# Kernel optimization log

Measured on AMD Instinct MI355X. Metric: run time of the kernel, lower is better.

Reference implementation:

```python
import jax, jax.numpy as jnp
import numpy as np

N_HEADS = 16
ROPE_THETA = 10000.0


def _rope(x):
    # x: (b, h, t, d). Interleaved-pair rotary embedding (lucidrains
    # rotary_embedding_torch convention: rotate_half on (d r) pairs, r=2).
    b, h, t, d = x.shape
    inv_freq = 1.0 / (ROPE_THETA ** (jnp.arange(0, d, 2, dtype=jnp.float32) / d))  # (d/2,)
    ang = jnp.arange(t, dtype=jnp.float32)[:, None] * inv_freq[None, :]            # (t, d/2)
    cos = jnp.cos(ang)
    sin = jnp.sin(ang)
    xp = x.reshape(b, h, t, d // 2, 2)
    x1, x2 = xp[..., 0], xp[..., 1]
    o1 = x1 * cos - x2 * sin
    o2 = x1 * sin + x2 * cos
    return jnp.stack([o1, o2], axis=-1).reshape(b, h, t, d)


def setup_inputs() -> dict:
    key = jax.random.key(0)
    k1, k2, k3 = jax.random.split(key, 3)
    B, T, C = 4, 2048, 1024
    x = jax.random.normal(k1, (B, T, C), dtype=jnp.float32)
    # torch nn.Linear weight layout: (out_features, in_features)
    w_attn = jax.random.normal(k2, (3 * C, C), dtype=jnp.float32) * (1.0 / np.sqrt(C))
    w_proj = jax.random.normal(k3, (C, C), dtype=jnp.float32) * (1.0 / np.sqrt(C))
    return {"x": x, "w_attn": w_attn, "w_proj": w_proj}


def reference(x, w_attn, w_proj):
    B, T, C = x.shape
    H = N_HEADS
    D = C // H
    # fused QKV projection: (b, t, 3C)
    qkv = jnp.einsum('btc,fc->btf', x, w_attn)
    # rearrange 'b t (r h d) -> r b h t d'
    qkv = qkv.reshape(B, T, 3, H, D).transpose(2, 0, 3, 1, 4)
    q, k, v = qkv[0], qkv[1], qkv[2]
    q = _rope(q)
    k = _rope(k)
    scale = 1.0 / np.sqrt(D).astype(np.float32)
    scores = jnp.einsum('bhqd,bhkd->bhqk', q, k) * scale
    attn = jax.nn.softmax(scores, axis=-1)
    y = jnp.einsum('bhqk,bhkd->bhqd', attn, v)       # (b, h, t, d)
    y = y.transpose(0, 2, 1, 3).reshape(B, T, C)     # 'b h t d -> b t (h d)'
    return jnp.einsum('btc,oc->bto', y, w_proj)
```

## Files before the change

### kernel.cpp

```cpp
#include <hip/hip_runtime.h>
#include <hip/hip_bf16.h>
#include <math.h>

typedef __bf16 bf16;
typedef float f32x4 __attribute__((ext_vector_type(4)));
typedef float f32x16 __attribute__((ext_vector_type(16)));
typedef bf16 bf16x8 __attribute__((ext_vector_type(8)));
typedef bf16 bf16x4 __attribute__((ext_vector_type(4)));
typedef unsigned int uint;
typedef uint uintx2 __attribute__((ext_vector_type(2)));

#define MFMA16(a, b, c) __builtin_amdgcn_mfma_f32_16x16x32_bf16(a, b, c, 0, 0, 0)
#define MFMA32(a, b, c) __builtin_amdgcn_mfma_f32_32x32x16_bf16(a, b, c, 0, 0, 0)

static constexpr int T_SEQ = 2048;
static constexpr int CDIM  = 1024;
static constexpr int NH    = 16;
static constexpr int DH    = 64;
static constexpr float FREQ_C = 0.20762050593045998f;
static constexpr float Q_SCALE = 0.18033688011112042f;

__device__ __forceinline__ float fexp2(float x) {
    return __builtin_amdgcn_exp2f(x);
}

__device__ __forceinline__ uint pack_bf16(float lo, float hi) {
    union { bf16 h[2]; uint u; } cv;
    cv.h[0] = (bf16)lo;
    cv.h[1] = (bf16)hi;
    return cv.u;
}

__device__ __forceinline__ void gld_lds16(const bf16* g, bf16* l) {
    __builtin_amdgcn_global_load_lds(
        (const __attribute__((address_space(1))) void*)g,
        (__attribute__((address_space(3))) void*)l, 16, 0, 0);
}

__device__ __forceinline__ void fast_sincos(float x, float* s, float* c) {
    const float INV2PI = 0.15915494309189535f;
    const float PI2_HI = 6.28125f;
    const float PI2_LO = 1.9353071795864769e-3f;
    const float n = rintf(x * INV2PI);
    float r = fmaf(-n, PI2_HI, x);
    r = fmaf(-n, PI2_LO, r);
    *s = __sinf(r);
    *c = __cosf(r);
}

__global__ __launch_bounds__(256)
void rope_table(float2* __restrict__ tab) {
    const int i = blockIdx.x * 256 + threadIdx.x;
    const int t = i >> 5, p = i & 31;
    const float ang = (float)t * exp2f(-2.0f * (float)p * FREQ_C);
    float s, c;
    fast_sincos(ang, &s, &c);
    tab[i] = make_float2(c, s);
}

__global__ __launch_bounds__(256)
void cvt_f32_bf16(const float* __restrict__ in, bf16* __restrict__ out, int n8) {
    const int i = blockIdx.x * 256 + threadIdx.x;
    if (i >= n8) return;
    const f32x4* p = (const f32x4*)(in + (size_t)i * 8);
    const f32x4 lo = p[0], hi = p[1];
    bf16x8 o;
    o[0] = (bf16)lo[0]; o[1] = (bf16)lo[1]; o[2] = (bf16)lo[2]; o[3] = (bf16)lo[3];
    o[4] = (bf16)hi[0]; o[5] = (bf16)hi[1]; o[6] = (bf16)hi[2]; o[7] = (bf16)hi[3];
    *(bf16x8*)(out + (size_t)i * 8) = o;
}

#define GEMM_CORE(Abase, Bbase, KDIM)                                            \
    f32x4 acc[4][4] = {};                                                        \
    for (int kk = 0; kk < (KDIM); kk += 64) {                                    \
        __syncthreads();                                                         \
        _Pragma("unroll")                                                        \
        for (int u = 0; u < 4; u++) {                                            \
            const int st = wave * 4 + u, mg = st >> 1, kg = st & 1;              \
            gld_lds16(Abase + (size_t)(mg * 16 + sm) * (KDIM) + kk + kg * 32 + sc * 8, \
                      &ash[st * 512]);                                           \
            gld_lds16(Bbase + (size_t)(mg * 16 + sm) * (KDIM) + kk + kg * 32 + sc * 8, \
                      &bsh[st * 512]);                                           \
        }                                                                        \
        __syncthreads();                                                         \
        _Pragma("unroll")                                                        \
        for (int kg = 0; kg < 2; kg++) {                                         \
            bf16x8 af[4], bfr[4];                                                \
            _Pragma("unroll")                                                    \
            for (int a = 0; a < 4; a++)                                          \
                af[a] = *(const bf16x8*)&ash[((wm * 4 + a) * 2 + kg) * 512 + lane * 8]; \
            _Pragma("unroll")                                                    \
            for (int b = 0; b < 4; b++)                                          \
                bfr[b] = *(const bf16x8*)&bsh[((wn * 4 + b) * 2 + kg) * 512 + lane * 8]; \
            _Pragma("unroll")                                                    \
            for (int a = 0; a < 4; a++)                                          \
                _Pragma("unroll")                                                \
                for (int b = 0; b < 4; b++)                                      \
                    acc[a][b] = MFMA16(af[a], bfr[b], acc[a][b]);                \
        }                                                                        \
    }

__global__ __launch_bounds__(256)
void gemm_qkv(const bf16* __restrict__ X, const bf16* __restrict__ W,
              bf16* __restrict__ Qo, bf16* __restrict__ Ko, bf16* __restrict__ Vt,
              const float2* __restrict__ tab) {
    __shared__ __align__(16) bf16 ash[16 * 512];
    __shared__ __align__(16) bf16 bsh[16 * 512];
    const int tid = threadIdx.x, lane = tid & 63, wave = tid >> 6;
    const int quad = lane >> 4, l16 = lane & 15;
    const int wm = wave >> 1, wn = wave & 1;
    const int lin = blockIdx.y * 24 + blockIdx.x;
    const int nl  = (lin & 7) * 192 + (lin >> 3);
    const int bm = nl / 24, bn = nl % 24;
    const int sm = lane & 15, sc = lane >> 4;

    const bf16* Abase = X + (size_t)(bm * 128) * CDIM;
    const bf16* Bbase = W + (size_t)(bn * 128) * CDIM;
    GEMM_CORE(Abase, Bbase, CDIM)

    const int rr    = (bn * 128) >> 10;
    const int nsec  = (bn * 128) & 1023;
    const int batch = (bm * 128) >> 11;
    const int tb    = ((bm * 128) & 2047) + wm * 64;

    if (rr == 2) {
#pragma unroll
        for (int b = 0; b < 4; b++) {
            const int n = nsec + wn * 64 + b * 16 + l16;
            const int h = n >> 6, d = n & 63;
            bf16* vp = Vt + ((size_t)(batch * NH + h) * DH + d) * T_SEQ;
#pragma unroll
            for (int a = 0; a < 4; a++) {
                const int t0 = tb + a * 16 + quad * 4;
                bf16x4 pk4 = { (bf16)acc[a][b][0], (bf16)acc[a][b][1],
                               (bf16)acc[a][b][2], (bf16)acc[a][b][3] };
                *(bf16x4*)(vp + t0) = pk4;
            }
        }
    } else {
        bf16* Dst = (rr == 0) ? Qo : Ko;
        const float scale = (rr == 0) ? Q_SCALE : 1.0f;
#pragma unroll
        for (int b = 0; b < 4; b++) {
            const int n = nsec + wn * 64 + b * 16 + l16;
            const int h = n >> 6, d = n & 63;
            const int p = d >> 1, odd = d & 1;
            bf16* dp = Dst + (size_t)(batch * NH + h) * T_SEQ * DH + d;
#pragma unroll
            for (int a = 0; a < 4; a++) {
#pragma unroll
                for (int r = 0; r < 4; r++) {
                    const int t = tb + a * 16 + quad * 4 + r;
                    const float val = acc[a][b][r];
                    const float partner = __shfl_xor(val, 1);
                    const float2 cs = tab[t * 32 + p];
                    float o = odd ? (partner * cs.y + val * cs.x)
                                  : (val * cs.x - partner * cs.y);
                    dp[(size_t)t * DH] = (bf16)(o * scale);
                }
            }
        }
    }
}

__global__ __launch_bounds__(256)
void gemm_proj(const bf16* __restrict__ X, const bf16* __restrict__ W,
               float* __restrict__ Out) {
    __shared__ __align__(16) bf16 ash[16 * 512];
    __shared__ __align__(16) bf16 bsh[16 * 512];
    const int tid = threadIdx.x, lane = tid & 63, wave = tid >> 6;
    const int quad = lane >> 4, l16 = lane & 15;
    const int wm = wave >> 1, wn = wave & 1;
    const int lin = blockIdx.y * 8 + blockIdx.x;
    const int nl  = (lin & 7) * 64 + (lin >> 3);
    const int bm = nl >> 3, bn = nl & 7;
    const int sm = lane & 15, sc = lane >> 4;

    const bf16* Abase = X + (size_t)(bm * 128) * CDIM;
    const bf16* Bbase = W + (size_t)(bn * 128) * CDIM;
    GEMM_CORE(Abase, Bbase, CDIM)

#pragma unroll
    for (int b = 0; b < 4; b++) {
        const int n = bn * 128 + wn * 64 + b * 16 + l16;
#pragma unroll
        for (int a = 0; a < 4; a++) {
            const int m = bm * 128 + wm * 64 + a * 16 + quad * 4;
#pragma unroll
            for (int r = 0; r < 4; r++)
                Out[(size_t)(m + r) * CDIM + n] = acc[a][b][r];
        }
    }
}

__global__ __launch_bounds__(256)
void flash(const bf16* __restrict__ Q, const bf16* __restrict__ K,
           const bf16* __restrict__ Vt, bf16* __restrict__ Y) {
    __shared__ __align__(16) bf16 ksh[2][8 * 512];
    __shared__ __align__(16) bf16 vsh[2][8 * 512];
    const int tid = threadIdx.x, lane = tid & 63, wave = tid >> 6;
    const int l32 = lane & 31, hi = lane >> 5;
    const int id = blockIdx.x;
    const int bh = (id & 7) * 8 + ((id >> 3) & 7);
    const int qsb = id >> 6;
    const size_t kbase = (size_t)bh * T_SEQ * DH;
    const size_t vbase = (size_t)bh * DH * T_SEQ;
    const int q0 = qsb * 256 + wave * 32;

    bf16x8 bq[2][4];
#pragma unroll
    for (int tq = 0; tq < 2; tq++) {
        const bf16* qp = Q + kbase + (size_t)(q0 + tq * 128 + l32) * DH + hi * 8;
#pragma unroll
        for (int c = 0; c < 4; c++) bq[tq][c] = *(const bf16x8*)(qp + c * 16);
    }

    f32x16 oT[2][2] = {};
    f32x16 lf[2] = {};
    bf16x8 onesf;
#pragma unroll
    for (int j = 0; j < 8; j++) onesf[j] = (bf16)1.0f;

#define STAGE(buf_, kt_) do {                                              \
        if (wave < 2) {                                                    \
            _Pragma("unroll")                                              \
            for (int u = 0; u < 4; u++) {                                  \
                const int s = wave * 4 + u, kb = s >> 2, c = s & 3;        \
                gld_lds16(K + kbase + (size_t)((kt_) + kb * 32 + l32) * DH \
                              + c * 16 + hi * 8,                           \
                          &ksh[buf_][s * 512]);                            \
            }                                                              \
        } else {                                                           \
            _Pragma("unroll")                                              \
            for (int u = 0; u < 4; u++) {                                  \
                const int s = (wave - 2) * 4 + u, db = s >> 2, kc = s & 3; \
                gld_lds16(Vt + vbase + (size_t)(db * 32 + l32) * T_SEQ     \
                              + (kt_) + kc * 16 + hi * 8,                  \
                          &vsh[buf_][s * 512]);                            \
            }                                                              \
        }                                                                  \
    } while (0)

    STAGE(0, 0);
    int ib = 0;
    for (int kt = 0; kt < T_SEQ; kt += 64, ib ^= 1) {
        __syncthreads();
        if (kt + 64 < T_SEQ) STAGE(ib ^ 1, kt + 64);

#pragma unroll
        for (int kb = 0; kb < 2; kb++) {
            f32x16 s0 = {}, s1 = {};
#pragma unroll
            for (int c = 0; c < 4; c++) {
                const bf16x8 a = *(const bf16x8*)&ksh[ib][(kb * 4 + c) * 512 + lane * 8];
                s0 = MFMA32(a, bq[0][c], s0);
                s1 = MFMA32(a, bq[1][c], s1);
            }
            uint P[2][8];
#pragma unroll
            for (int w = 0; w < 8; w++) {
                P[0][w] = pack_bf16(fexp2(s0[2 * w]), fexp2(s0[2 * w + 1]));
                P[1][w] = pack_bf16(fexp2(s1[2 * w]), fexp2(s1[2 * w + 1]));
            }
#pragma unroll
            for (int t = 0; t < 2; t++) {
                const int kc = kb * 2 + t;
                bf16x8 vv[2];
#pragma unroll
                for (int db = 0; db < 2; db++)
                    vv[db] = *(const bf16x8*)&vsh[ib][(db * 4 + kc) * 512 + lane * 8];
#pragma unroll
                for (int tq = 0; tq < 2; tq++) {
                    const uintx2 rA = __builtin_amdgcn_permlane32_swap(
                        P[tq][4 * t + 0], P[tq][4 * t + 2], false, false);
                    const uintx2 rB = __builtin_amdgcn_permlane32_swap(
                        P[tq][4 * t + 1], P[tq][4 * t + 3], false, false);
                    union { uint u[4]; bf16x8 v; } bP;
                    bP.u[0] = rA[0]; bP.u[1] = rB[0];
                    bP.u[2] = rA[1]; bP.u[3] = rB[1];
                    lf[tq] = MFMA32(onesf, bP.v, lf[tq]);
#pragma unroll
                    for (int db = 0; db < 2; db++)
                        oT[tq][db] = MFMA32(vv[db], bP.v, oT[tq][db]);
                }
            }
        }
    }
#undef STAGE

    const int b = bh >> 4, h = bh & 15;
#pragma unroll
    for (int tq = 0; tq < 2; tq++) {
        const float inv = 1.0f / lf[tq][0];
        const size_t yrow =
            ((size_t)b * T_SEQ + q0 + tq * 128 + l32) * CDIM + h * DH;
#pragma unroll
        for (int db = 0; db < 2; db++)
#pragma unroll
            for (int rg = 0; rg < 4; rg++) {
                bf16x4 o4 = { (bf16)(oT[tq][db][rg * 4 + 0] * inv),
                              (bf16)(oT[tq][db][rg * 4 + 1] * inv),
                              (bf16)(oT[tq][db][rg * 4 + 2] * inv),
                              (bf16)(oT[tq][db][rg * 4 + 3] * inv) };
                *(bf16x4*)(Y + yrow + db * 32 + 8 * rg + 4 * hi) = o4;
            }
    }
}

extern "C" void kernel_launch(void* const* d_in, const int* in_sizes, int n_in,
                              void* d_out, int out_size, void* d_ws, size_t ws_size,
                              hipStream_t stream) {
    const float* x      = (const float*)d_in[0];
    const float* w_attn = (const float*)d_in[1];
    const float* w_proj = (const float*)d_in[2];
    float* out = (float*)d_out;

    bf16* ws = (bf16*)d_ws;
    const size_t SZ = (size_t)4 * NH * T_SEQ * DH;
    bf16* Xb  = ws;
    bf16* Wab = Xb + SZ;
    bf16* Wpb = Wab + 3145728;
    bf16* Qb  = Wpb + 1048576;
    bf16* Kb  = Qb + SZ;
    bf16* Vtb = Kb + SZ;
    bf16* Yb  = Vtb + SZ;
    float2* tab = (float2*)(Yb + SZ);

    rope_table<<<256, 256, 0, stream>>>(tab);
    cvt_f32_bf16<<<4096, 256, 0, stream>>>(x, Xb, 1048576);
    cvt_f32_bf16<<<1536, 256, 0, stream>>>(w_attn, Wab, 393216);
    cvt_f32_bf16<<<512, 256, 0, stream>>>(w_proj, Wpb, 131072);

    gemm_qkv<<<dim3(24, 64), 256, 0, stream>>>(Xb, Wab, Qb, Kb, Vtb, tab);
    flash<<<512, 256, 0, stream>>>(Qb, Kb, Vtb, Yb);
    gemm_proj<<<dim3(8, 64), 256, 0, stream>>>(Yb, Wpb, out);
}
```

Measured before the change: 322.8 us.

## Prefetch next GEMM tile into LDS during MFMA and preload attention K/V fragments

The GEMM loop now reads LDS fragments into registers up front, then issues the next k-tile's global-to-LDS loads before running the MFMAs. This overlaps global memory latency with compute while keeping a single LDS buffer. The attention loop likewise loads all K/V fragments into registers before staging the next tile, with a sched_barrier to fix the ordering. Block-to-tile mapping in both GEMMs is also changed to group M-tiles per XCD for better L2 locality. In exchange, register pressure rises.

```diff
diff --git a/kernel.cpp b/kernel.cpp
--- a/kernel.cpp
+++ b/kernel.cpp
@@ -70,34 +70,41 @@
     *(bf16x8*)(out + (size_t)i * 8) = o;
 }
 
-#define GEMM_CORE(Abase, Bbase, KDIM)                                            \
-    f32x4 acc[4][4] = {};                                                        \
-    for (int kk = 0; kk < (KDIM); kk += 64) {                                    \
-        __syncthreads();                                                         \
+#define GEMM_STAGE(kk_, Abase, Bbase, KDIM) do {                                 \
         _Pragma("unroll")                                                        \
         for (int u = 0; u < 4; u++) {                                            \
             const int st = wave * 4 + u, mg = st >> 1, kg = st & 1;              \
-            gld_lds16(Abase + (size_t)(mg * 16 + sm) * (KDIM) + kk + kg * 32 + sc * 8, \
+            gld_lds16((Abase) + (size_t)(mg * 16 + sm) * (KDIM) + (kk_) + kg * 32 + sc * 8, \
                       &ash[st * 512]);                                           \
-            gld_lds16(Bbase + (size_t)(mg * 16 + sm) * (KDIM) + kk + kg * 32 + sc * 8, \
+            gld_lds16((Bbase) + (size_t)(mg * 16 + sm) * (KDIM) + (kk_) + kg * 32 + sc * 8, \
                       &bsh[st * 512]);                                           \
         }                                                                        \
-        __syncthreads();                                                         \
+    } while (0)
+
+#define GEMM_CORE(Abase, Bbase, KDIM)                                            \
+    f32x4 acc[4][4] = {};                                                        \
+    GEMM_STAGE(0, Abase, Bbase, KDIM);                                           \
+    for (int kk = 0; kk < (KDIM); kk += 64) {                                    \
+        __syncthreads();                        \
+        bf16x8 af[2][4], bfr[2][4];                                              \
         _Pragma("unroll")                                                        \
-        for (int kg = 0; kg < 2; kg++) {                                         \
-            bf16x8 af[4], bfr[4];                                                \
+        for (int kg = 0; kg < 2; kg++)                                           \
             _Pragma("unroll")                                                    \
-            for (int a = 0; a < 4; a++)                                          \
-                af[a] = *(const bf16x8*)&ash[((wm * 4 + a) * 2 + kg) * 512 + lane * 8]; \
-            _Pragma("unroll")                                                    \
-            for (int b = 0; b < 4; b++)                                          \
-                bfr[b] = *(const bf16x8*)&bsh[((wn * 4 + b) * 2 + kg) * 512 + lane * 8]; \
+            for (int a = 0; a < 4; a++) {                                        \
+                af[kg][a]  = *(const bf16x8*)&ash[((wm * 4 + a) * 2 + kg) * 512 + lane * 8]; \
+                bfr[kg][a] = *(const bf16x8*)&bsh[((wn * 4 + a) * 2 + kg) * 512 + lane * 8]; \
+            }                                                                    \
+        __syncthreads();                   \
+        if (kk + 64 < (KDIM))                                                    \
+            GEMM_STAGE(kk + 64, Abase, Bbase, KDIM);                             \
+        __builtin_amdgcn_sched_barrier(0);                                       \
+        _Pragma("unroll")                                                        \
+        for (int kg = 0; kg < 2; kg++)                                           \
             _Pragma("unroll")                                                    \
             for (int a = 0; a < 4; a++)                                          \
                 _Pragma("unroll")                                                \
                 for (int b = 0; b < 4; b++)                                      \
-                    acc[a][b] = MFMA16(af[a], bfr[b], acc[a][b]);                \
-        }                                                                        \
+                    acc[a][b] = MFMA16(af[kg][a], bfr[kg][b], acc[a][b]);        \
     }
 
 __global__ __launch_bounds__(256)
@@ -110,8 +117,8 @@
     const int quad = lane >> 4, l16 = lane & 15;
     const int wm = wave >> 1, wn = wave & 1;
     const int lin = blockIdx.y * 24 + blockIdx.x;
-    const int nl  = (lin & 7) * 192 + (lin >> 3);
-    const int bm = nl / 24, bn = nl % 24;
+    const int xcd = lin & 7, j = lin >> 3;
+    const int bm = xcd * 8 + (j & 7), bn = j >> 3;
     const int sm = lane & 15, sc = lane >> 4;
 
     const bf16* Abase = X + (size_t)(bm * 128) * CDIM;
@@ -172,8 +179,8 @@
     const int quad = lane >> 4, l16 = lane & 15;
     const int wm = wave >> 1, wn = wave & 1;
     const int lin = blockIdx.y * 8 + blockIdx.x;
-    const int nl  = (lin & 7) * 64 + (lin >> 3);
-    const int bm = nl >> 3, bn = nl & 7;
+    const int xcd = lin & 7, j = lin >> 3;
+    const int bm = xcd * 8 + (j & 7), bn = j >> 3;
     const int sm = lane & 15, sc = lane >> 4;
 
     const bf16* Abase = X + (size_t)(bm * 128) * CDIM;
@@ -245,16 +252,22 @@
     int ib = 0;
     for (int kt = 0; kt < T_SEQ; kt += 64, ib ^= 1) {
         __syncthreads();
+        bf16x8 kf[8], vf[8];
+#pragma unroll
+        for (int i = 0; i < 8; i++) {
+            kf[i] = *(const bf16x8*)&ksh[ib][i * 512 + lane * 8];
+            vf[i] = *(const bf16x8*)&vsh[ib][i * 512 + lane * 8];
+        }
         if (kt + 64 < T_SEQ) STAGE(ib ^ 1, kt + 64);
+        __builtin_amdgcn_sched_barrier(0);
 
 #pragma unroll
         for (int kb = 0; kb < 2; kb++) {
             f32x16 s0 = {}, s1 = {};
 #pragma unroll
             for (int c = 0; c < 4; c++) {
-                const bf16x8 a = *(const bf16x8*)&ksh[ib][(kb * 4 + c) * 512 + lane * 8];
-                s0 = MFMA32(a, bq[0][c], s0);
-                s1 = MFMA32(a, bq[1][c], s1);
+                s0 = MFMA32(kf[kb * 4 + c], bq[0][c], s0);
+                s1 = MFMA32(kf[kb * 4 + c], bq[1][c], s1);
             }
             uint P[2][8];
 #pragma unroll
@@ -265,10 +278,6 @@
 #pragma unroll
             for (int t = 0; t < 2; t++) {
                 const int kc = kb * 2 + t;
-                bf16x8 vv[2];
-#pragma unroll
-                for (int db = 0; db < 2; db++)
-                    vv[db] = *(const bf16x8*)&vsh[ib][(db * 4 + kc) * 512 + lane * 8];
 #pragma unroll
                 for (int tq = 0; tq < 2; tq++) {
                     const uintx2 rA = __builtin_amdgcn_permlane32_swap(
@@ -281,7 +290,7 @@
                     lf[tq] = MFMA32(onesf, bP.v, lf[tq]);
 #pragma unroll
                     for (int db = 0; db < 2; db++)
-                        oT[tq][db] = MFMA32(vv[db], bP.v, oT[tq][db]);
+                        oT[tq][db] = MFMA32(vf[db * 4 + kc], bP.v, oT[tq][db]);
                 }
             }
         }
```

Measured after the change: 330.8 us. 2.5% more time.

## Enlarge GEMM tiles to 256x128 so each B tile is reused across two A tiles

Applied to the files above, without the earlier changes.

Both the QKV and output projection GEMMs now compute a 256x128 output tile per block: two 128-row A tiles share one B tile in shared memory, and each wave accumulates 32 MFMA tiles instead of 16. This raises arithmetic intensity and halves the number of blocks and B loads. The block-to-XCD mapping is reworked to fit the new grid. In exchange, accumulator register pressure doubles and shared memory grows to 48KB, which may reduce occupancy. The smaller grid (256 blocks for proj) may also underfill the GPU.

```diff
diff --git a/kernel.cpp b/kernel.cpp
--- a/kernel.cpp
+++ b/kernel.cpp
@@ -70,33 +70,40 @@
     *(bf16x8*)(out + (size_t)i * 8) = o;
 }
 
-#define GEMM_CORE(Abase, Bbase, KDIM)                                            \
-    f32x4 acc[4][4] = {};                                                        \
-    for (int kk = 0; kk < (KDIM); kk += 64) {                                    \
-        __syncthreads();                                                         \
+#define GEMM_STAGE2(kk_, A0, A1, Bb, KDIM) do {                                  \
         _Pragma("unroll")                                                        \
         for (int u = 0; u < 4; u++) {                                            \
             const int st = wave * 4 + u, mg = st >> 1, kg = st & 1;              \
-            gld_lds16(Abase + (size_t)(mg * 16 + sm) * (KDIM) + kk + kg * 32 + sc * 8, \
-                      &ash[st * 512]);                                           \
-            gld_lds16(Bbase + (size_t)(mg * 16 + sm) * (KDIM) + kk + kg * 32 + sc * 8, \
-                      &bsh[st * 512]);                                           \
+            const size_t off = (size_t)(mg * 16 + sm) * (KDIM) + (kk_)           \
+                               + kg * 32 + sc * 8;                               \
+            gld_lds16((A0) + off, &ash0[st * 512]);                              \
+            gld_lds16((A1) + off, &ash1[st * 512]);                              \
+            gld_lds16((Bb) + off, &bsh[st * 512]);                               \
         }                                                                        \
+    } while (0)
+
+#define GEMM_CORE2(A0, A1, Bb, KDIM)                                             \
+    f32x4 acc[2][4][4] = {};                                                     \
+    for (int kk = 0; kk < (KDIM); kk += 64) {                                    \
+        __syncthreads();                                                         \
+        GEMM_STAGE2(kk, A0, A1, Bb, KDIM);                                       \
         __syncthreads();                                                         \
         _Pragma("unroll")                                                        \
         for (int kg = 0; kg < 2; kg++) {                                         \
-            bf16x8 af[4], bfr[4];                                                \
+            bf16x8 af0[4], af1[4], bfr[4];                                       \
             _Pragma("unroll")                                                    \
-            for (int a = 0; a < 4; a++)                                          \
-                af[a] = *(const bf16x8*)&ash[((wm * 4 + a) * 2 + kg) * 512 + lane * 8]; \
-            _Pragma("unroll")                                                    \
-            for (int b = 0; b < 4; b++)                                          \
-                bfr[b] = *(const bf16x8*)&bsh[((wn * 4 + b) * 2 + kg) * 512 + lane * 8]; \
+            for (int a = 0; a < 4; a++) {                                        \
+                af0[a] = *(const bf16x8*)&ash0[((wm * 4 + a) * 2 + kg) * 512 + lane * 8]; \
+                af1[a] = *(const bf16x8*)&ash1[((wm * 4 + a) * 2 + kg) * 512 + lane * 8]; \
+                bfr[a] = *(const bf16x8*)&bsh[((wn * 4 + a) * 2 + kg) * 512 + lane * 8];  \
+            }                                                                    \
             _Pragma("unroll")                                                    \
             for (int a = 0; a < 4; a++)                                          \
                 _Pragma("unroll")                                                \
-                for (int b = 0; b < 4; b++)                                      \
-                    acc[a][b] = MFMA16(af[a], bfr[b], acc[a][b]);                \
+                for (int b = 0; b < 4; b++) {                                    \
+                    acc[0][a][b] = MFMA16(af0[a], bfr[b], acc[0][a][b]);         \
+                    acc[1][a][b] = MFMA16(af1[a], bfr[b], acc[1][a][b]);         \
+                }                                                                \
         }                                                                        \
     }
 
@@ -104,59 +111,66 @@
 void gemm_qkv(const bf16* __restrict__ X, const bf16* __restrict__ W,
               bf16* __restrict__ Qo, bf16* __restrict__ Ko, bf16* __restrict__ Vt,
               const float2* __restrict__ tab) {
-    __shared__ __align__(16) bf16 ash[16 * 512];
+    __shared__ __align__(16) bf16 ash0[16 * 512];
+    __shared__ __align__(16) bf16 ash1[16 * 512];
     __shared__ __align__(16) bf16 bsh[16 * 512];
     const int tid = threadIdx.x, lane = tid & 63, wave = tid >> 6;
     const int quad = lane >> 4, l16 = lane & 15;
     const int wm = wave >> 1, wn = wave & 1;
     const int lin = blockIdx.y * 24 + blockIdx.x;
-    const int nl  = (lin & 7) * 192 + (lin >> 3);
-    const int bm = nl / 24, bn = nl % 24;
+    const int xcd = lin & 7, j = lin >> 3;
+    const int bmp = xcd * 4 + (j & 3), bn = j >> 2;
     const int sm = lane & 15, sc = lane >> 4;
 
-    const bf16* Abase = X + (size_t)(bm * 128) * CDIM;
-    const bf16* Bbase = W + (size_t)(bn * 128) * CDIM;
-    GEMM_CORE(Abase, Bbase, CDIM)
+    const bf16* A0 = X + (size_t)(bmp * 256) * CDIM;
+    const bf16* A1 = A0 + (size_t)128 * CDIM;
+    const bf16* Bb = W + (size_t)(bn * 128) * CDIM;
+    GEMM_CORE2(A0, A1, Bb, CDIM)
 
     const int rr    = (bn * 128) >> 10;
     const int nsec  = (bn * 128) & 1023;
-    const int batch = (bm * 128) >> 11;
-    const int tb    = ((bm * 128) & 2047) + wm * 64;
-
-    if (rr == 2) {
-#pragma unroll
-        for (int b = 0; b < 4; b++) {
-            const int n = nsec + wn * 64 + b * 16 + l16;
-            const int h = n >> 6, d = n & 63;
-            bf16* vp = Vt + ((size_t)(batch * NH + h) * DH + d) * T_SEQ;
-#pragma unroll
-            for (int a = 0; a < 4; a++) {
-                const int t0 = tb + a * 16 + quad * 4;
-                bf16x4 pk4 = { (bf16)acc[a][b][0], (bf16)acc[a][b][1],
-                               (bf16)acc[a][b][2], (bf16)acc[a][b][3] };
-                *(bf16x4*)(vp + t0) = pk4;
-            }
-        }
-    } else {
-        bf16* Dst = (rr == 0) ? Qo : Ko;
-        const float scale = (rr == 0) ? Q_SCALE : 1.0f;
-#pragma unroll
-        for (int b = 0; b < 4; b++) {
-            const int n = nsec + wn * 64 + b * 16 + l16;
-            const int h = n >> 6, d = n & 63;
-            const int p = d >> 1, odd = d & 1;
-            bf16* dp = Dst + (size_t)(batch * NH + h) * T_SEQ * DH + d;
-#pragma unroll
-            for (int a = 0; a < 4; a++) {
-#pragma unroll
-                for (int r = 0; r < 4; r++) {
-                    const int t = tb + a * 16 + quad * 4 + r;
-                    const float val = acc[a][b][r];
-                    const float partner = __shfl_xor(val, 1);
-                    const float2 cs = tab[t * 32 + p];
-                    float o = odd ? (partner * cs.y + val * cs.x)
-                                  : (val * cs.x - partner * cs.y);
-                    dp[(size_t)t * DH] = (bf16)(o * scale);
+
+#pragma unroll
+    for (int tt = 0; tt < 2; tt++) {
+        const int bm_eff = bmp * 2 + tt;
+        const int batch = (bm_eff * 128) >> 11;
+        const int tb    = ((bm_eff * 128) & 2047) + wm * 64;
+
+        if (rr == 2) {
+#pragma unroll
+            for (int b = 0; b < 4; b++) {
+                const int n = nsec + wn * 64 + b * 16 + l16;
+                const int h = n >> 6, d = n & 63;
+                bf16* vp = Vt + ((size_t)(batch * NH + h) * DH + d) * T_SEQ;
+#pragma unroll
+                for (int a = 0; a < 4; a++) {
+                    const int t0 = tb + a * 16 + quad * 4;
+                    bf16x4 pk4 = { (bf16)acc[tt][a][b][0], (bf16)acc[tt][a][b][1],
+                                   (bf16)acc[tt][a][b][2], (bf16)acc[tt][a][b][3] };
+                    *(bf16x4*)(vp + t0) = pk4;
+                }
+            }
+        } else {
+            bf16* Dst = (rr == 0) ? Qo : Ko;
+            const float scale = (rr == 0) ? Q_SCALE : 1.0f;
+#pragma unroll
+            for (int b = 0; b < 4; b++) {
+                const int n = nsec + wn * 64 + b * 16 + l16;
+                const int h = n >> 6, d = n & 63;
+                const int p = d >> 1, odd = d & 1;
+                bf16* dp = Dst + (size_t)(batch * NH + h) * T_SEQ * DH + d;
+#pragma unroll
+                for (int a = 0; a < 4; a++) {
+#pragma unroll
+                    for (int r = 0; r < 4; r++) {
+                        const int t = tb + a * 16 + quad * 4 + r;
+                        const float val = acc[tt][a][b][r];
+                        const float partner = __shfl_xor(val, 1);
+                        const float2 cs = tab[t * 32 + p];
+                        float o = odd ? (partner * cs.y + val * cs.x)
+                                      : (val * cs.x - partner * cs.y);
+                        dp[(size_t)t * DH] = (bf16)(o * scale);
+                    }
                 }
             }
         }
@@ -166,29 +180,34 @@
 __global__ __launch_bounds__(256)
 void gemm_proj(const bf16* __restrict__ X, const bf16* __restrict__ W,
                float* __restrict__ Out) {
-    __shared__ __align__(16) bf16 ash[16 * 512];
+    __shared__ __align__(16) bf16 ash0[16 * 512];
+    __shared__ __align__(16) bf16 ash1[16 * 512];
     __shared__ __align__(16) bf16 bsh[16 * 512];
     const int tid = threadIdx.x, lane = tid & 63, wave = tid >> 6;
     const int quad = lane >> 4, l16 = lane & 15;
     const int wm = wave >> 1, wn = wave & 1;
     const int lin = blockIdx.y * 8 + blockIdx.x;
-    const int nl  = (lin & 7) * 64 + (lin >> 3);
-    const int bm = nl >> 3, bn = nl & 7;
+    const int xcd = lin & 7, j = lin >> 3;
+    const int bmp = xcd * 4 + (j & 3), bn = j >> 2;
     const int sm = lane & 15, sc = lane >> 4;
 
-    const bf16* Abase = X + (size_t)(bm * 128) * CDIM;
-    const bf16* Bbase = W + (size_t)(bn * 128) * CDIM;
-    GEMM_CORE(Abase, Bbase, CDIM)
-
-#pragma unroll
-    for (int b = 0; b < 4; b++) {
-        const int n = bn * 128 + wn * 64 + b * 16 + l16;
-#pragma unroll
-        for (int a = 0; a < 4; a++) {
-            const int m = bm * 128 + wm * 64 + a * 16 + quad * 4;
-#pragma unroll
-            for (int r = 0; r < 4; r++)
-                Out[(size_t)(m + r) * CDIM + n] = acc[a][b][r];
+    const bf16* A0 = X + (size_t)(bmp * 256) * CDIM;
+    const bf16* A1 = A0 + (size_t)128 * CDIM;
+    const bf16* Bb = W + (size_t)(bn * 128) * CDIM;
+    GEMM_CORE2(A0, A1, Bb, CDIM)
+
+#pragma unroll
+    for (int tt = 0; tt < 2; tt++) {
+#pragma unroll
+        for (int b = 0; b < 4; b++) {
+            const int n = bn * 128 + wn * 64 + b * 16 + l16;
+#pragma unroll
+            for (int a = 0; a < 4; a++) {
+                const int m = (bmp * 2 + tt) * 128 + wm * 64 + a * 16 + quad * 4;
+#pragma unroll
+                for (int r = 0; r < 4; r++)
+                    Out[(size_t)(m + r) * CDIM + n] = acc[tt][a][b][r];
+            }
         }
     }
 }
@@ -331,7 +350,7 @@
     cvt_f32_bf16<<<1536, 256, 0, stream>>>(w_attn, Wab, 393216);
     cvt_f32_bf16<<<512, 256, 0, stream>>>(w_proj, Wpb, 131072);
 
-    gemm_qkv<<<dim3(24, 64), 256, 0, stream>>>(Xb, Wab, Qb, Kb, Vtb, tab);
+    gemm_qkv<<<dim3(24, 32), 256, 0, stream>>>(Xb, Wab, Qb, Kb, Vtb, tab);
     flash<<<512, 256, 0, stream>>>(Qb, Kb, Vtb, Yb);
-    gemm_proj<<<dim3(8, 64), 256, 0, stream>>>(Yb, Wpb, out);
-}
+    gemm_proj<<<dim3(8, 32), 256, 0, stream>>>(Yb, Wpb, out);
+}
```

Result: slower. 363.2 us (+12.5%).
